# Kernel optimization log

Hardware: AMD Instinct MI355X
Metric: run time of the kernel (lower is better)

Reference implementation:

```python
import jax, jax.numpy as jnp
import numpy as np

CD_WEIGHT = 1.0
EMD_WEIGHT = 1.0
EPS = 1e-3        # sinkhorn entropic regularization (matches eps=0.001)
ITERS = 50        # matches max_iters=50 (stop_thresh ignored: fixed trip count for jit)
NEG = -1e9        # log(0) stand-in for padded points
BIG = 1e10        # +inf stand-in for masked chamfer distances


def _sqdist(x, y):
    # x [N,3], y [M,3] -> squared euclidean distances [N,M]  (p=2 cost)
    return jnp.maximum(
        jnp.sum(x * x, -1)[:, None] + jnp.sum(y * y, -1)[None, :] - 2.0 * (x @ y.T),
        0.0,
    )


def _sinkhorn_cost(x, y, n, m):
    # Log-domain Sinkhorn OT cost between one padded pair: x [N,3], y [M,3],
    # with n, m valid points and uniform marginals 1/n, 1/m on valid points.
    N, M = x.shape[0], y.shape[0]
    C = _sqdist(x, y)
    nf = n.astype(jnp.float32)
    mf = m.astype(jnp.float32)
    log_a = jnp.where(jnp.arange(N) < n, -jnp.log(nf), NEG)  # [N]
    log_b = jnp.where(jnp.arange(M) < m, -jnp.log(mf), NEG)  # [M]

    def body(_, fg):
        f, g = fg
        f = -EPS * jax.scipy.special.logsumexp(log_b[None, :] + (g[None, :] - C) / EPS, axis=1)
        g = -EPS * jax.scipy.special.logsumexp(log_a[:, None] + (f[:, None] - C) / EPS, axis=0)
        return (f, g)

    f, g = jax.lax.fori_loop(0, ITERS, body, (jnp.zeros(N), jnp.zeros(M)))
    log_P = log_a[:, None] + log_b[None, :] + (f[:, None] + g[None, :] - C) / EPS
    return jnp.sum(jnp.exp(log_P) * C)


def _chamfer(px, gy, n_len, m_len):
    # pytorch3d chamfer_distance with point_reduction='mean', batch_reduction='mean'
    # px [B,N,3], gy [B,M,3]; n_len/m_len [B] float valid counts.
    B, N, _ = px.shape
    M = gy.shape[1]
    D = jnp.maximum(
        jnp.sum(px * px, -1)[:, :, None]
        + jnp.sum(gy * gy, -1)[:, None, :]
        - 2.0 * jnp.einsum('bnd,bmd->bnm', px, gy),
        0.0,
    )  # [B,N,M]
    mx = jnp.arange(N)[None, :] < n_len[:, None]  # [B,N]
    my = jnp.arange(M)[None, :] < m_len[:, None]  # [B,M]
    dx = jnp.min(jnp.where(my[:, None, :], D, BIG), axis=2)  # [B,N] NN dist x->y
    dy = jnp.min(jnp.where(mx[:, :, None], D, BIG), axis=1)  # [B,M] NN dist y->x
    cham_x = jnp.sum(jnp.where(mx, dx, 0.0), axis=1) / n_len.astype(jnp.float32)
    cham_y = jnp.sum(jnp.where(my, dy, 0.0), axis=1) / m_len.astype(jnp.float32)
    return jnp.mean(cham_x + cham_y)


def setup_inputs() -> dict:
    key = jax.random.key(0)
    k1, k2, k3, k4 = jax.random.split(key, 4)
    B, N, M = 8, 2048, 2048
    pred_points = 0.5 * jax.random.normal(k1, (B, N, 3), dtype=jnp.float32)
    gt_points = 0.5 * jax.random.normal(k2, (B, M, 3), dtype=jnp.float32)
    pred_lengths = jax.random.randint(k3, (B,), N // 2, N + 1, dtype=jnp.int32)
    gt_lengths = jax.random.randint(k4, (B,), M // 2, M + 1, dtype=jnp.int32)
    return {
        'pred_points': pred_points,
        'gt_points': gt_points,
        'pred_lengths': pred_lengths,
        'gt_lengths': gt_lengths,
    }


def reference(pred_points, gt_points, pred_lengths, gt_lengths):
    # Original clips extracted points to [-1, 1] before losses.
    px = jnp.clip(pred_points, -1.0, 1.0)
    gy = jnp.clip(gt_points, -1.0, 1.0)
    # EMD: per-sample sinkhorn cost, sqrt, mean over samples, weighted.
    emd_costs = jax.vmap(_sinkhorn_cost)(px, gy, pred_lengths, gt_lengths)  # [B]
    emd_loss = EMD_WEIGHT * jnp.mean(jnp.sqrt(emd_costs))
    # Chamfer on padded clouds with lengths.
    cd_loss = CD_WEIGHT * _chamfer(px, gy, pred_lengths.astype(jnp.float32), gt_lengths.astype(jnp.float32))
    return cd_loss + emd_loss
```

## Files before the change

### kernel.cpp

```cpp
#include <hip/hip_runtime.h>

#define BATCH 8
#define NPTS  2048
#define TPB   512
#define WGB   64
#define NWG   (BATCH*WGB)
#define ITERS 50
#define R     4

#define KLOG2E    1442.6950408889634f
#define TWO_K     2885.3900817779268f
#define INV_TK    3.4657359027997264e-4f
#define INV_K     6.931471805599453e-4f
#define INV_2K_SQ 1.2011325347955035e-7f
#define AR_SCALE  -1.7328679513998632e-4f
#define EPS_LN2   6.931471805599453e-4f
#define LN2       0.6931471805599453f
#define EPSV      1e-3f
#define NEGU      -1e30f
#define BIGD      1e10f

__device__ __forceinline__ float exp2fast(float x) { return __builtin_amdgcn_exp2f(x); }
__device__ __forceinline__ float log2fast(float x) { return __builtin_amdgcn_logf(x); }
__device__ __forceinline__ float clipf(float v)    { return fminf(fmaxf(v, -1.0f), 1.0f); }

__device__ __forceinline__ float aloadf(const float* p) {
    return __hip_atomic_load(p, __ATOMIC_RELAXED, __HIP_MEMORY_SCOPE_AGENT);
}
__device__ __forceinline__ void astoref(float* p, float v) {
    __hip_atomic_store(p, v, __ATOMIC_RELAXED, __HIP_MEMORY_SCOPE_AGENT);
}
__device__ __forceinline__ int aloadi(const int* p) {
    return __hip_atomic_load(p, __ATOMIC_RELAXED, __HIP_MEMORY_SCOPE_AGENT);
}

__device__ __forceinline__ float wsum(float v) {
#pragma unroll
    for (int d = 1; d < 64; d <<= 1) v += __shfl_xor(v, d);
    return v;
}
__device__ __forceinline__ float wmax(float v) {
#pragma unroll
    for (int d = 1; d < 64; d <<= 1) v = fmaxf(v, __shfl_xor(v, d));
    return v;
}
__device__ __forceinline__ float wmin(float v) {
#pragma unroll
    for (int d = 1; d < 64; d <<= 1) v = fminf(v, __shfl_xor(v, d));
    return v;
}

__device__ __forceinline__ void batch_barrier(int* cnt, int* gen, int tid)
{
    __syncthreads();
    if (tid == 0) {
        asm volatile("s_waitcnt vmcnt(0)" ::: "memory");
        int g = aloadi(gen);
        int a = __hip_atomic_fetch_add(cnt, 1, __ATOMIC_RELAXED, __HIP_MEMORY_SCOPE_AGENT);
        if (a == WGB - 1) {
            __hip_atomic_store(cnt, 0, __ATOMIC_RELAXED, __HIP_MEMORY_SCOPE_AGENT);
            asm volatile("s_waitcnt vmcnt(0)" ::: "memory");
            __hip_atomic_store(gen, g + 1, __ATOMIC_RELAXED, __HIP_MEMORY_SCOPE_AGENT);
        } else {
            while (aloadi(gen) == g) __builtin_amdgcn_s_sleep(1);
        }
    }
    __syncthreads();
}

__device__ __forceinline__ void half_fused(const float4* __restrict__ colbuf,
                                           const float4* __restrict__ rowbuf,
                                           float* __restrict__ outv,
                                           float* L, float* D,
                                           int nrows, int ncols, float eln,
                                           int r0, int lane)
{
    if (r0 >= nrows) return;
    const int nst = (ncols + 63) >> 6;
    const float4* cb = colbuf + lane;

    float x0[R], x1[R], x2[R], ar[R], Lp[R];
#pragma unroll
    for (int r = 0; r < R; ++r) {
        float4 s = rowbuf[r0 + r];
        x0[r] = s.x * INV_TK; x1[r] = s.y * INV_TK; x2[r] = s.z * INV_TK;
        ar[r] = AR_SCALE * fmaf(s.x, s.x, fmaf(s.y, s.y, s.z * s.z));
        Lp[r] = L[r] + D[r];
    }

    float S[R];
#pragma unroll
    for (int r = 0; r < R; ++r) S[r] = 0.0f;
#pragma unroll 2
    for (int s = 0; s < nst; ++s) {
        float4 yb = cb[s << 6];
#pragma unroll
        for (int r = 0; r < R; ++r) {
            float t = fmaf(x0[r], yb.x, fmaf(x1[r], yb.y, fmaf(x2[r], yb.z, yb.w)));
            S[r] += exp2fast(t - Lp[r]);
        }
    }
    float Ssum[R];
    bool redo = false;
#pragma unroll
    for (int r = 0; r < R; ++r) {
        Ssum[r] = wsum(S[r]);
        redo |= !(Ssum[r] >= 1e-30f && Ssum[r] <= 1e30f);
    }
    if (redo) {
        float Mn[R];
#pragma unroll
        for (int r = 0; r < R; ++r) Mn[r] = -3.0e38f;
        for (int s = 0; s < nst; ++s) {
            float4 yb = cb[s << 6];
#pragma unroll
            for (int r = 0; r < R; ++r) {
                float t = fmaf(x0[r], yb.x, fmaf(x1[r], yb.y, fmaf(x2[r], yb.z, yb.w)));
                Mn[r] = fmaxf(Mn[r], t);
            }
        }
#pragma unroll
        for (int r = 0; r < R; ++r) { Lp[r] = wmax(Mn[r]); S[r] = 0.0f; }
        for (int s = 0; s < nst; ++s) {
            float4 yb = cb[s << 6];
#pragma unroll
            for (int r = 0; r < R; ++r) {
                float t = fmaf(x0[r], yb.x, fmaf(x1[r], yb.y, fmaf(x2[r], yb.z, yb.w)));
                S[r] += exp2fast(t - Lp[r]);
            }
        }
#pragma unroll
        for (int r = 0; r < R; ++r) Ssum[r] = wsum(S[r]);
    }

    float fv[R];
#pragma unroll
    for (int r = 0; r < R; ++r) {
        float lnew = Lp[r] + log2fast(Ssum[r]);
        D[r] = (L[r] > 1.0e37f) ? 0.0f : (lnew - L[r]);
        L[r] = lnew;
        fv[r] = fmaf(-EPS_LN2, ar[r] + lnew, eln);
    }
    float v = fv[0];
#pragma unroll
    for (int r = 1; r < R; ++r) v = (lane == r) ? fv[r] : v;
    if (lane < R && (r0 + lane) < nrows) astoref(&outv[r0 + lane], v);
}

__launch_bounds__(TPB, 4)
__global__ void pcl_kernel(const float* __restrict__ pred,
                           const float* __restrict__ gt,
                           const int* __restrict__ nlen,
                           const int* __restrict__ mlen,
                           int* __restrict__ hdr,
                           float* __restrict__ fbuf,
                           float* __restrict__ gbuf,
                           float* __restrict__ parts,
                           float* __restrict__ bres,
                           float* __restrict__ out)
{
    __shared__ float4 xbuf[NPTS];
    __shared__ float4 ybuf[NPTS];

    const int tid  = threadIdx.x;
    const int wg   = blockIdx.x;
    const int lo   = wg & 255;
    const int hi   = wg >> 8;
    const int b    = ((lo & 7) + hi) & 7;
    const int wloc = (lo >> 3) + hi * 32;
    const int wv   = tid >> 6;
    const int lane = tid & 63;
    const int r0   = wloc * 32 + wv * R;
    const int n = nlen[b];
    const int m = mlen[b];
    const float nf = (float)n, mf = (float)m;
    const float* predb = pred + (size_t)b * NPTS * 3;
    const float* gtb   = gt   + (size_t)b * NPTS * 3;
    float* fb = fbuf + b * NPTS;
    float* gb = gbuf + b * NPTS;
    int* cnt  = hdr + b * 16;
    int* gen  = hdr + 128 + b * 16;
    int* done = hdr + 256;

    for (int idx = tid; idx < NPTS; idx += TPB) {
        const float* p = predb + (size_t)idx * 3;
        xbuf[idx] = make_float4(clipf(p[0]) * TWO_K, clipf(p[1]) * TWO_K, clipf(p[2]) * TWO_K, 0.0f);
        const float* q = gtb + (size_t)idx * 3;
        ybuf[idx] = make_float4(clipf(q[0]) * TWO_K, clipf(q[1]) * TWO_K, clipf(q[2]) * TWO_K, 0.0f);
    }

    const float eln_m = EPSV * LN2 * log2fast(mf);
    const float eln_n = EPSV * LN2 * log2fast(nf);

    float Lf[R], Lg[R], Df[R], Dg[R];
#pragma unroll
    for (int r = 0; r < R; ++r) {
        Lf[r] = 3.0e38f; Lg[r] = 3.0e38f;
        Df[r] = 0.0f;    Dg[r] = 0.0f;
    }

    for (int it = 0; it < ITERS; ++it) {
        for (int j = tid; j < NPTS; j += TPB) {
            float4 yb = ybuf[j];
            float yy = fmaf(yb.x, yb.x, fmaf(yb.y, yb.y, yb.z * yb.z)) * INV_2K_SQ;
            float gval = (it == 0) ? 0.0f : aloadf(&gb[j]);
            ybuf[j].w = (j < m) ? (gval - yy) * KLOG2E : NEGU;
        }
        __syncthreads();
        half_fused(ybuf, xbuf, fb, Lf, Df, n, m, eln_m, r0, lane);
        batch_barrier(cnt, gen, tid);
        for (int i = tid; i < NPTS; i += TPB) {
            float4 xb = xbuf[i];
            float xx = fmaf(xb.x, xb.x, fmaf(xb.y, xb.y, xb.z * xb.z)) * INV_2K_SQ;
            xbuf[i].w = (i < n) ? (aloadf(&fb[i]) - xx) * KLOG2E : NEGU;
        }
        __syncthreads();
        half_fused(xbuf, ybuf, gb, Lg, Dg, m, n, eln_n, r0, lane);
        batch_barrier(cnt, gen, tid);
    }

    for (int j = tid; j < NPTS; j += TPB) {
        float4 yb = ybuf[j];
        float yy = fmaf(yb.x, yb.x, fmaf(yb.y, yb.y, yb.z * yb.z)) * INV_2K_SQ;
        ybuf[j].w = (j < m) ? (aloadf(&gb[j]) - yy) * KLOG2E : NEGU;
    }
    __syncthreads();

    float wcost = 0.0f, chx = 0.0f;
    if (r0 < n) {
        float px0[R], px1[R], px2[R], pxx[R], hrow[R], dmn[R];
#pragma unroll
        for (int r = 0; r < R; ++r) {
            float4 s = xbuf[r0 + r];
            px0[r] = s.x * INV_TK; px1[r] = s.y * INV_TK; px2[r] = s.z * INV_TK;
            pxx[r] = fmaf(s.x, s.x, fmaf(s.y, s.y, s.z * s.z)) * INV_2K_SQ;
            hrow[r] = (r0 + r < n) ? (aloadf(&fb[r0 + r]) - pxx[r]) * KLOG2E : NEGU;
            dmn[r] = BIGD;
        }
        const int nst = (m + 63) >> 6;
#pragma unroll 2
        for (int s = 0; s < nst; ++s) {
            int jj = (s << 6) + lane;
            float4 yb = ybuf[jj];
            float yy = fmaf(yb.x, yb.x, fmaf(yb.y, yb.y, yb.z * yb.z)) * INV_2K_SQ;
            bool jv = jj < m;
#pragma unroll
            for (int r = 0; r < R; ++r) {
                float dots = fmaf(px0[r], yb.x, fmaf(px1[r], yb.y, px2[r] * yb.z));
                float e = hrow[r] + yb.w + dots;
                float w = exp2fast(e);
                float C = fmaxf(fmaf(dots, -INV_K, pxx[r] + yy), 0.0f);
                wcost = fmaf(w, C, wcost);
                dmn[r] = fminf(dmn[r], jv ? C : BIGD);
            }
        }
#pragma unroll
        for (int r = 0; r < R; ++r) {
            float d = wmin(dmn[r]);
            if (r0 + r < n) chx += d;
        }
        wcost = wsum(wcost);
    }

    float chy = 0.0f;
    if (r0 < m) {
        float qy0[R], qy1[R], qy2[R], qyy[R], dmn[R];
#pragma unroll
        for (int r = 0; r < R; ++r) {
            float4 s = ybuf[r0 + r];
            qy0[r] = s.x * INV_TK; qy1[r] = s.y * INV_TK; qy2[r] = s.z * INV_TK;
            qyy[r] = fmaf(s.x, s.x, fmaf(s.y, s.y, s.z * s.z)) * INV_2K_SQ;
            dmn[r] = BIGD;
        }
        const int nst = (n + 63) >> 6;
#pragma unroll 2
        for (int s = 0; s < nst; ++s) {
            int ii = (s << 6) + lane;
            float4 xb = xbuf[ii];
            float xx = fmaf(xb.x, xb.x, fmaf(xb.y, xb.y, xb.z * xb.z)) * INV_2K_SQ;
            bool iv = ii < n;
#pragma unroll
            for (int r = 0; r < R; ++r) {
                float dots = fmaf(qy0[r], xb.x, fmaf(qy1[r], xb.y, qy2[r] * xb.z));
                float C = fmaxf(fmaf(dots, -INV_K, qyy[r] + xx), 0.0f);
                dmn[r] = fminf(dmn[r], iv ? C : BIGD);
            }
        }
#pragma unroll
        for (int r = 0; r < R; ++r) {
            float d = wmin(dmn[r]);
            if (r0 + r < m) chy += d;
        }
    }
    __syncthreads();

    float* xs = (float*)xbuf;
    if (lane == 0) { xs[wv] = wcost; xs[8 + wv] = chx; xs[16 + wv] = chy; }
    __syncthreads();
    if (tid == 0) {
        float cs = 0.0f, cx = 0.0f, cy = 0.0f;
        for (int w = 0; w < 8; ++w) { cs += xs[w]; cx += xs[8 + w]; cy += xs[16 + w]; }
        astoref(&parts[(b * WGB + wloc) * 4 + 0], cs);
        astoref(&parts[(b * WGB + wloc) * 4 + 1], cx);
        astoref(&parts[(b * WGB + wloc) * 4 + 2], cy);
    }
    batch_barrier(cnt, gen, tid);

    if (wloc == 0 && wv == 0) {
        float cs = aloadf(&parts[(b * WGB + lane) * 4 + 0]);
        float cx = aloadf(&parts[(b * WGB + lane) * 4 + 1]);
        float cy = aloadf(&parts[(b * WGB + lane) * 4 + 2]);
        cs = wsum(cs); cx = wsum(cx); cy = wsum(cy);
        if (lane == 0) {
            float cost = cs / (nf * mf);
            astoref(&bres[b], sqrtf(fmaxf(cost, 0.0f)) + cx / nf + cy / mf);
            asm volatile("s_waitcnt vmcnt(0)" ::: "memory");
            int a = __hip_atomic_fetch_add(done, 1, __ATOMIC_RELAXED, __HIP_MEMORY_SCOPE_AGENT);
            if (a == BATCH - 1) {
                float acc = 0.0f;
                for (int i2 = 0; i2 < BATCH; ++i2) acc += aloadf(&bres[i2]);
                out[0] = acc * 0.125f;
            }
        }
    }
}

extern "C" void kernel_launch(void* const* d_in, const int* in_sizes, int n_in,
                              void* d_out, int out_size, void* d_ws, size_t ws_size,
                              hipStream_t stream) {
    const float* pred = (const float*)d_in[0];
    const float* gt   = (const float*)d_in[1];
    const int*  nlen  = (const int*)d_in[2];
    const int*  mlen  = (const int*)d_in[3];

    int*   hdr   = (int*)d_ws;
    float* base  = (float*)d_ws + 512;
    float* fbuf  = base;
    float* gbuf  = fbuf + BATCH * NPTS;
    float* parts = gbuf + BATCH * NPTS;
    float* bres  = parts + NWG * 4;
    float* out   = (float*)d_out;

    hipMemsetAsync(d_ws, 0, 2048, stream);
    hipLaunchKernelGGL(pcl_kernel, dim3(NWG), dim3(TPB), 0, stream,
                       pred, gt, nlen, mlen, hdr, fbuf, gbuf, parts, bres, out);
}
```

Measured before the change: 835.9 us.

## Use packed FP32 math with SoA shared layout and hierarchical batch barrier

Shared point buffers move from float4 AoS to split x/y/z/w arrays of float2, so the inner Sinkhorn loop can use v_pk_fma_f32/v_pk_add_f32 and handle two columns per lane per step. The dual potentials are now stored directly in the log2-scaled domain, which drops the per-iteration rescaling of the column weights. The per-batch grid barrier becomes a two-level tree (8 sub-counters feeding a top counter) to cut contention on a single atomic. Chamfer loops are also converted to paired-column processing. The risks are inline asm that blocks compiler scheduling, higher register pressure, and a more complex barrier.

```diff
diff --git a/kernel.cpp b/kernel.cpp
--- a/kernel.cpp
+++ b/kernel.cpp
@@ -14,15 +14,26 @@
 #define INV_K     6.931471805599453e-4f
 #define INV_2K_SQ 1.2011325347955035e-7f
 #define AR_SCALE  -1.7328679513998632e-4f
-#define EPS_LN2   6.931471805599453e-4f
-#define LN2       0.6931471805599453f
-#define EPSV      1e-3f
 #define NEGU      -1e30f
 #define BIGD      1e10f
+
+typedef float f2 __attribute__((ext_vector_type(2)));
 
 __device__ __forceinline__ float exp2fast(float x) { return __builtin_amdgcn_exp2f(x); }
 __device__ __forceinline__ float log2fast(float x) { return __builtin_amdgcn_logf(x); }
 __device__ __forceinline__ float clipf(float v)    { return fminf(fmaxf(v, -1.0f), 1.0f); }
+__device__ __forceinline__ f2 bc(float x) { f2 r; r.x = x; r.y = x; return r; }
+
+__device__ __forceinline__ f2 pk_fma(f2 a, f2 b, f2 c) {
+    f2 d;
+    asm("v_pk_fma_f32 %0, %1, %2, %3" : "=v"(d) : "v"(a), "v"(b), "v"(c));
+    return d;
+}
+__device__ __forceinline__ f2 pk_add(f2 a, f2 b) {
+    f2 d;
+    asm("v_pk_add_f32 %0, %1, %2" : "=v"(d) : "v"(a), "v"(b));
+    return d;
+}
 
 __device__ __forceinline__ float aloadf(const float* p) {
     return __hip_atomic_load(p, __ATOMIC_RELAXED, __HIP_MEMORY_SCOPE_AGENT);
@@ -33,6 +44,9 @@
 __device__ __forceinline__ int aloadi(const int* p) {
     return __hip_atomic_load(p, __ATOMIC_RELAXED, __HIP_MEMORY_SCOPE_AGENT);
 }
+__device__ __forceinline__ void astorei(int* p, int v) {
+    __hip_atomic_store(p, v, __ATOMIC_RELAXED, __HIP_MEMORY_SCOPE_AGENT);
+}
 
 __device__ __forceinline__ float wsum(float v) {
 #pragma unroll
@@ -50,17 +64,25 @@
     return v;
 }
 
-__device__ __forceinline__ void batch_barrier(int* cnt, int* gen, int tid)
+__device__ __forceinline__ void batch_barrier(int* subs_base, int* sub, int* top,
+                                              int* gen, int tid)
 {
     __syncthreads();
     if (tid == 0) {
         asm volatile("s_waitcnt vmcnt(0)" ::: "memory");
         int g = aloadi(gen);
-        int a = __hip_atomic_fetch_add(cnt, 1, __ATOMIC_RELAXED, __HIP_MEMORY_SCOPE_AGENT);
-        if (a == WGB - 1) {
-            __hip_atomic_store(cnt, 0, __ATOMIC_RELAXED, __HIP_MEMORY_SCOPE_AGENT);
-            asm volatile("s_waitcnt vmcnt(0)" ::: "memory");
-            __hip_atomic_store(gen, g + 1, __ATOMIC_RELAXED, __HIP_MEMORY_SCOPE_AGENT);
+        int a = __hip_atomic_fetch_add(sub, 1, __ATOMIC_RELAXED, __HIP_MEMORY_SCOPE_AGENT);
+        if (a == 7) {
+            int t = __hip_atomic_fetch_add(top, 1, __ATOMIC_RELAXED, __HIP_MEMORY_SCOPE_AGENT);
+            if (t == 7) {
+#pragma unroll
+                for (int s = 0; s < 8; ++s) astorei(subs_base + s * 16, 0);
+                astorei(top, 0);
+                asm volatile("s_waitcnt vmcnt(0)" ::: "memory");
+                astorei(gen, g + 1);
+            } else {
+                while (aloadi(gen) == g) __builtin_amdgcn_s_sleep(1);
+            }
         } else {
             while (aloadi(gen) == g) __builtin_amdgcn_s_sleep(1);
         }
@@ -68,43 +90,51 @@
     __syncthreads();
 }
 
-__device__ __forceinline__ void half_fused(const float4* __restrict__ colbuf,
-                                           const float4* __restrict__ rowbuf,
-                                           float* __restrict__ outv,
-                                           float* L, float* D,
-                                           int nrows, int ncols, float eln,
-                                           int r0, int lane)
+__device__ __forceinline__ void half_fused_pk(
+    const f2* __restrict__ cx, const f2* __restrict__ cy,
+    const f2* __restrict__ cz, const f2* __restrict__ cw,
+    const f2* __restrict__ rx, const f2* __restrict__ ry, const f2* __restrict__ rz,
+    float* __restrict__ uout, float L2C, float* L, float* D,
+    int nrows, int ncols, int r0, int lane)
 {
     if (r0 >= nrows) return;
-    const int nst = (ncols + 63) >> 6;
-    const float4* cb = colbuf + lane;
-
-    float x0[R], x1[R], x2[R], ar[R], Lp[R];
-#pragma unroll
-    for (int r = 0; r < R; ++r) {
-        float4 s = rowbuf[r0 + r];
-        x0[r] = s.x * INV_TK; x1[r] = s.y * INV_TK; x2[r] = s.z * INV_TK;
-        ar[r] = AR_SCALE * fmaf(s.x, s.x, fmaf(s.y, s.y, s.z * s.z));
-        Lp[r] = L[r] + D[r];
-    }
-
-    float S[R];
-#pragma unroll
-    for (int r = 0; r < R; ++r) S[r] = 0.0f;
-#pragma unroll 2
+    const int nst = (ncols + 127) >> 7;
+    const int rp = r0 >> 1;
+    f2 vx0 = rx[rp], vx1 = rx[rp + 1];
+    f2 vy0 = ry[rp], vy1 = ry[rp + 1];
+    f2 vz0 = rz[rp], vz1 = rz[rp + 1];
+    f2 x0p[R] = { bc(vx0.x * INV_TK), bc(vx0.y * INV_TK), bc(vx1.x * INV_TK), bc(vx1.y * INV_TK) };
+    f2 x1p[R] = { bc(vy0.x * INV_TK), bc(vy0.y * INV_TK), bc(vy1.x * INV_TK), bc(vy1.y * INV_TK) };
+    f2 x2p[R] = { bc(vz0.x * INV_TK), bc(vz0.y * INV_TK), bc(vz1.x * INV_TK), bc(vz1.y * INV_TK) };
+
+    float Lp[R];
+    f2 nLp[R];
+#pragma unroll
+    for (int r = 0; r < R; ++r) { Lp[r] = L[r] + D[r]; nLp[r] = bc(-Lp[r]); }
+
+    float S0[R], S1[R];
+#pragma unroll
+    for (int r = 0; r < R; ++r) { S0[r] = 0.0f; S1[r] = 0.0f; }
+
     for (int s = 0; s < nst; ++s) {
-        float4 yb = cb[s << 6];
-#pragma unroll
-        for (int r = 0; r < R; ++r) {
-            float t = fmaf(x0[r], yb.x, fmaf(x1[r], yb.y, fmaf(x2[r], yb.z, yb.w)));
-            S[r] += exp2fast(t - Lp[r]);
-        }
-    }
+        int p = (s << 6) + lane;
+        f2 bx = cx[p], by = cy[p], bz = cz[p], bw = cw[p];
+#pragma unroll
+        for (int r = 0; r < R; ++r) {
+            f2 t = pk_fma(x2p[r], bz, bw);
+            t = pk_fma(x1p[r], by, t);
+            t = pk_fma(x0p[r], bx, t);
+            t = pk_add(nLp[r], t);
+            S0[r] += exp2fast(t.x);
+            S1[r] += exp2fast(t.y);
+        }
+    }
+
     float Ssum[R];
     bool redo = false;
 #pragma unroll
     for (int r = 0; r < R; ++r) {
-        Ssum[r] = wsum(S[r]);
+        Ssum[r] = wsum(S0[r] + S1[r]);
         redo |= !(Ssum[r] >= 1e-30f && Ssum[r] <= 1e30f);
     }
     if (redo) {
@@ -112,39 +142,50 @@
 #pragma unroll
         for (int r = 0; r < R; ++r) Mn[r] = -3.0e38f;
         for (int s = 0; s < nst; ++s) {
-            float4 yb = cb[s << 6];
+            int p = (s << 6) + lane;
+            f2 bx = cx[p], by = cy[p], bz = cz[p], bw = cw[p];
 #pragma unroll
             for (int r = 0; r < R; ++r) {
-                float t = fmaf(x0[r], yb.x, fmaf(x1[r], yb.y, fmaf(x2[r], yb.z, yb.w)));
-                Mn[r] = fmaxf(Mn[r], t);
-            }
-        }
-#pragma unroll
-        for (int r = 0; r < R; ++r) { Lp[r] = wmax(Mn[r]); S[r] = 0.0f; }
+                f2 t = pk_fma(x2p[r], bz, bw);
+                t = pk_fma(x1p[r], by, t);
+                t = pk_fma(x0p[r], bx, t);
+                Mn[r] = fmaxf(Mn[r], fmaxf(t.x, t.y));
+            }
+        }
+#pragma unroll
+        for (int r = 0; r < R; ++r) {
+            Lp[r] = wmax(Mn[r]); nLp[r] = bc(-Lp[r]);
+            S0[r] = 0.0f; S1[r] = 0.0f;
+        }
         for (int s = 0; s < nst; ++s) {
-            float4 yb = cb[s << 6];
+            int p = (s << 6) + lane;
+            f2 bx = cx[p], by = cy[p], bz = cz[p], bw = cw[p];
 #pragma unroll
             for (int r = 0; r < R; ++r) {
-                float t = fmaf(x0[r], yb.x, fmaf(x1[r], yb.y, fmaf(x2[r], yb.z, yb.w)));
-                S[r] += exp2fast(t - Lp[r]);
-            }
-        }
-#pragma unroll
-        for (int r = 0; r < R; ++r) Ssum[r] = wsum(S[r]);
-    }
-
-    float fv[R];
+                f2 t = pk_fma(x2p[r], bz, bw);
+                t = pk_fma(x1p[r], by, t);
+                t = pk_fma(x0p[r], bx, t);
+                t = pk_add(nLp[r], t);
+                S0[r] += exp2fast(t.x);
+                S1[r] += exp2fast(t.y);
+            }
+        }
+#pragma unroll
+        for (int r = 0; r < R; ++r) Ssum[r] = wsum(S0[r] + S1[r]);
+    }
+
+    float uv[R];
 #pragma unroll
     for (int r = 0; r < R; ++r) {
         float lnew = Lp[r] + log2fast(Ssum[r]);
         D[r] = (L[r] > 1.0e37f) ? 0.0f : (lnew - L[r]);
         L[r] = lnew;
-        fv[r] = fmaf(-EPS_LN2, ar[r] + lnew, eln);
-    }
-    float v = fv[0];
-#pragma unroll
-    for (int r = 1; r < R; ++r) v = (lane == r) ? fv[r] : v;
-    if (lane < R && (r0 + lane) < nrows) astoref(&outv[r0 + lane], v);
+        uv[r] = L2C - lnew;
+    }
+    float v = uv[0];
+#pragma unroll
+    for (int r = 1; r < R; ++r) v = (lane == r) ? uv[r] : v;
+    if (lane < R && (r0 + lane) < nrows) astoref(&uout[r0 + lane], v);
 }
 
 __launch_bounds__(TPB, 4)
@@ -159,8 +200,8 @@
                            float* __restrict__ bres,
                            float* __restrict__ out)
 {
-    __shared__ float4 xbuf[NPTS];
-    __shared__ float4 ybuf[NPTS];
+    __shared__ f2 XSX[NPTS/2], XSY[NPTS/2], XSZ[NPTS/2], XSW[NPTS/2];
+    __shared__ f2 YSX[NPTS/2], YSY[NPTS/2], YSZ[NPTS/2], YSW[NPTS/2];
 
     const int tid  = threadIdx.x;
     const int wg   = blockIdx.x;
@@ -178,19 +219,26 @@
     const float* gtb   = gt   + (size_t)b * NPTS * 3;
     float* fb = fbuf + b * NPTS;
     float* gb = gbuf + b * NPTS;
-    int* cnt  = hdr + b * 16;
-    int* gen  = hdr + 128 + b * 16;
-    int* done = hdr + 256;
+    int* subs_base = hdr + b * 128;
+    int* sub       = subs_base + (wloc >> 3) * 16;
+    int* top       = hdr + (64 + b) * 16;
+    int* gen       = hdr + (72 + b) * 16;
+    int* done      = hdr + 80 * 16;
 
     for (int idx = tid; idx < NPTS; idx += TPB) {
         const float* p = predb + (size_t)idx * 3;
-        xbuf[idx] = make_float4(clipf(p[0]) * TWO_K, clipf(p[1]) * TWO_K, clipf(p[2]) * TWO_K, 0.0f);
+        ((float*)XSX)[idx] = clipf(p[0]) * TWO_K;
+        ((float*)XSY)[idx] = clipf(p[1]) * TWO_K;
+        ((float*)XSZ)[idx] = clipf(p[2]) * TWO_K;
         const float* q = gtb + (size_t)idx * 3;
-        ybuf[idx] = make_float4(clipf(q[0]) * TWO_K, clipf(q[1]) * TWO_K, clipf(q[2]) * TWO_K, 0.0f);
-    }
-
-    const float eln_m = EPSV * LN2 * log2fast(mf);
-    const float eln_n = EPSV * LN2 * log2fast(nf);
+        ((float*)YSX)[idx] = clipf(q[0]) * TWO_K;
+        ((float*)YSY)[idx] = clipf(q[1]) * TWO_K;
+        ((float*)YSZ)[idx] = clipf(q[2]) * TWO_K;
+    }
+    __syncthreads();
+
+    const float L2M = log2fast(mf);
+    const float L2N = log2fast(nf);
 
     float Lf[R], Lg[R], Df[R], Dg[R];
 #pragma unroll
@@ -200,63 +248,71 @@
     }
 
     for (int it = 0; it < ITERS; ++it) {
-        for (int j = tid; j < NPTS; j += TPB) {
-            float4 yb = ybuf[j];
-            float yy = fmaf(yb.x, yb.x, fmaf(yb.y, yb.y, yb.z * yb.z)) * INV_2K_SQ;
-            float gval = (it == 0) ? 0.0f : aloadf(&gb[j]);
-            ybuf[j].w = (j < m) ? (gval - yy) * KLOG2E : NEGU;
+        if (it == 0) {
+            for (int j = tid; j < NPTS; j += TPB) {
+                float sx = ((float*)YSX)[j], sy = ((float*)YSY)[j], sz = ((float*)YSZ)[j];
+                float u0 = AR_SCALE * fmaf(sx, sx, fmaf(sy, sy, sz * sz));
+                ((float*)YSW)[j] = (j < m) ? u0 : NEGU;
+            }
+        } else {
+            for (int j = tid; j < NPTS; j += TPB)
+                ((float*)YSW)[j] = (j < m) ? aloadf(&gb[j]) : NEGU;
         }
         __syncthreads();
-        half_fused(ybuf, xbuf, fb, Lf, Df, n, m, eln_m, r0, lane);
-        batch_barrier(cnt, gen, tid);
-        for (int i = tid; i < NPTS; i += TPB) {
-            float4 xb = xbuf[i];
-            float xx = fmaf(xb.x, xb.x, fmaf(xb.y, xb.y, xb.z * xb.z)) * INV_2K_SQ;
-            xbuf[i].w = (i < n) ? (aloadf(&fb[i]) - xx) * KLOG2E : NEGU;
-        }
+        half_fused_pk(YSX, YSY, YSZ, YSW, XSX, XSY, XSZ, fb, L2M, Lf, Df, n, m, r0, lane);
+        batch_barrier(subs_base, sub, top, gen, tid);
+        for (int i = tid; i < NPTS; i += TPB)
+            ((float*)XSW)[i] = (i < n) ? aloadf(&fb[i]) : NEGU;
         __syncthreads();
-        half_fused(xbuf, ybuf, gb, Lg, Dg, m, n, eln_n, r0, lane);
-        batch_barrier(cnt, gen, tid);
-    }
-
-    for (int j = tid; j < NPTS; j += TPB) {
-        float4 yb = ybuf[j];
-        float yy = fmaf(yb.x, yb.x, fmaf(yb.y, yb.y, yb.z * yb.z)) * INV_2K_SQ;
-        ybuf[j].w = (j < m) ? (aloadf(&gb[j]) - yy) * KLOG2E : NEGU;
-    }
+        half_fused_pk(XSX, XSY, XSZ, XSW, YSX, YSY, YSZ, gb, L2N, Lg, Dg, m, n, r0, lane);
+        batch_barrier(subs_base, sub, top, gen, tid);
+    }
+
+    for (int j = tid; j < NPTS; j += TPB)
+        ((float*)YSW)[j] = (j < m) ? aloadf(&gb[j]) : NEGU;
     __syncthreads();
 
     float wcost = 0.0f, chx = 0.0f;
     if (r0 < n) {
-        float px0[R], px1[R], px2[R], pxx[R], hrow[R], dmn[R];
-#pragma unroll
-        for (int r = 0; r < R; ++r) {
-            float4 s = xbuf[r0 + r];
-            px0[r] = s.x * INV_TK; px1[r] = s.y * INV_TK; px2[r] = s.z * INV_TK;
-            pxx[r] = fmaf(s.x, s.x, fmaf(s.y, s.y, s.z * s.z)) * INV_2K_SQ;
-            hrow[r] = (r0 + r < n) ? (aloadf(&fb[r0 + r]) - pxx[r]) * KLOG2E : NEGU;
-            dmn[r] = BIGD;
-        }
-        const int nst = (m + 63) >> 6;
-#pragma unroll 2
+        const int rp = r0 >> 1;
+        f2 vx0 = XSX[rp], vx1 = XSX[rp + 1];
+        f2 vy0 = XSY[rp], vy1 = XSY[rp + 1];
+        f2 vz0 = XSZ[rp], vz1 = XSZ[rp + 1];
+        float px0[R] = { vx0.x * INV_TK, vx0.y * INV_TK, vx1.x * INV_TK, vx1.y * INV_TK };
+        float px1[R] = { vy0.x * INV_TK, vy0.y * INV_TK, vy1.x * INV_TK, vy1.y * INV_TK };
+        float px2[R] = { vz0.x * INV_TK, vz0.y * INV_TK, vz1.x * INV_TK, vz1.y * INV_TK };
+        float pxx[R], hrow[R];
+        f2 dmn[R];
+#pragma unroll
+        for (int r = 0; r < R; ++r) {
+            float sx = px0[r] * TWO_K, sy = px1[r] * TWO_K, sz = px2[r] * TWO_K;
+            pxx[r] = fmaf(sx, sx, fmaf(sy, sy, sz * sz)) * INV_2K_SQ;
+            hrow[r] = (r0 + r < n) ? aloadf(&fb[r0 + r]) : NEGU;
+            dmn[r].x = BIGD; dmn[r].y = BIGD;
+        }
+        const int nst = (m + 127) >> 7;
         for (int s = 0; s < nst; ++s) {
-            int jj = (s << 6) + lane;
-            float4 yb = ybuf[jj];
-            float yy = fmaf(yb.x, yb.x, fmaf(yb.y, yb.y, yb.z * yb.z)) * INV_2K_SQ;
-            bool jv = jj < m;
+            int p = (s << 6) + lane;
+            f2 bx = YSX[p], by = YSY[p], bz = YSZ[p], bw = YSW[p];
+            f2 yy2 = (bx * bx + by * by + bz * bz) * INV_2K_SQ;
+            bool jv0 = (2 * p)     < m;
+            bool jv1 = (2 * p + 1) < m;
 #pragma unroll
             for (int r = 0; r < R; ++r) {
-                float dots = fmaf(px0[r], yb.x, fmaf(px1[r], yb.y, px2[r] * yb.z));
-                float e = hrow[r] + yb.w + dots;
-                float w = exp2fast(e);
-                float C = fmaxf(fmaf(dots, -INV_K, pxx[r] + yy), 0.0f);
-                wcost = fmaf(w, C, wcost);
-                dmn[r] = fminf(dmn[r], jv ? C : BIGD);
-            }
-        }
-#pragma unroll
-        for (int r = 0; r < R; ++r) {
-            float d = wmin(dmn[r]);
+                f2 dots = px0[r] * bx + px1[r] * by + px2[r] * bz;
+                f2 e = dots + bw + hrow[r];
+                float w0 = exp2fast(e.x), w1 = exp2fast(e.y);
+                f2 C;
+                C.x = fmaxf(fmaf(dots.x, -INV_K, pxx[r] + yy2.x), 0.0f);
+                C.y = fmaxf(fmaf(dots.y, -INV_K, pxx[r] + yy2.y), 0.0f);
+                wcost = fmaf(w0, C.x, fmaf(w1, C.y, wcost));
+                dmn[r].x = fminf(dmn[r].x, jv0 ? C.x : BIGD);
+                dmn[r].y = fminf(dmn[r].y, jv1 ? C.y : BIGD);
+            }
+        }
+#pragma unroll
+        for (int r = 0; r < R; ++r) {
+            float d = wmin(fminf(dmn[r].x, dmn[r].y));
             if (r0 + r < n) chx += d;
         }
         wcost = wsum(wcost);
@@ -264,37 +320,47 @@
 
     float chy = 0.0f;
     if (r0 < m) {
-        float qy0[R], qy1[R], qy2[R], qyy[R], dmn[R];
-#pragma unroll
-        for (int r = 0; r < R; ++r) {
-            float4 s = ybuf[r0 + r];
-            qy0[r] = s.x * INV_TK; qy1[r] = s.y * INV_TK; qy2[r] = s.z * INV_TK;
-            qyy[r] = fmaf(s.x, s.x, fmaf(s.y, s.y, s.z * s.z)) * INV_2K_SQ;
-            dmn[r] = BIGD;
-        }
-        const int nst = (n + 63) >> 6;
-#pragma unroll 2
+        const int rp = r0 >> 1;
+        f2 vx0 = YSX[rp], vx1 = YSX[rp + 1];
+        f2 vy0 = YSY[rp], vy1 = YSY[rp + 1];
+        f2 vz0 = YSZ[rp], vz1 = YSZ[rp + 1];
+        float qy0[R] = { vx0.x * INV_TK, vx0.y * INV_TK, vx1.x * INV_TK, vx1.y * INV_TK };
+        float qy1[R] = { vy0.x * INV_TK, vy0.y * INV_TK, vy1.x * INV_TK, vy1.y * INV_TK };
+        float qy2[R] = { vz0.x * INV_TK, vz0.y * INV_TK, vz1.x * INV_TK, vz1.y * INV_TK };
+        float qyy[R];
+        f2 dmn[R];
+#pragma unroll
+        for (int r = 0; r < R; ++r) {
+            float sx = qy0[r] * TWO_K, sy = qy1[r] * TWO_K, sz = qy2[r] * TWO_K;
+            qyy[r] = fmaf(sx, sx, fmaf(sy, sy, sz * sz)) * INV_2K_SQ;
+            dmn[r].x = BIGD; dmn[r].y = BIGD;
+        }
+        const int nst = (n + 127) >> 7;
         for (int s = 0; s < nst; ++s) {
-            int ii = (s << 6) + lane;
-            float4 xb = xbuf[ii];
-            float xx = fmaf(xb.x, xb.x, fmaf(xb.y, xb.y, xb.z * xb.z)) * INV_2K_SQ;
-            bool iv = ii < n;
+            int p = (s << 6) + lane;
+            f2 bx = XSX[p], by = XSY[p], bz = XSZ[p];
+            f2 xx2 = (bx * bx + by * by + bz * bz) * INV_2K_SQ;
+            bool iv0 = (2 * p)     < n;
+            bool iv1 = (2 * p + 1) < n;
 #pragma unroll
             for (int r = 0; r < R; ++r) {
-                float dots = fmaf(qy0[r], xb.x, fmaf(qy1[r], xb.y, qy2[r] * xb.z));
-                float C = fmaxf(fmaf(dots, -INV_K, qyy[r] + xx), 0.0f);
-                dmn[r] = fminf(dmn[r], iv ? C : BIGD);
-            }
-        }
-#pragma unroll
-        for (int r = 0; r < R; ++r) {
-            float d = wmin(dmn[r]);
+                f2 dots = qy0[r] * bx + qy1[r] * by + qy2[r] * bz;
+                f2 C;
+                C.x = fmaxf(fmaf(dots.x, -INV_K, qyy[r] + xx2.x), 0.0f);
+                C.y = fmaxf(fmaf(dots.y, -INV_K, qyy[r] + xx2.y), 0.0f);
+                dmn[r].x = fminf(dmn[r].x, iv0 ? C.x : BIGD);
+                dmn[r].y = fminf(dmn[r].y, iv1 ? C.y : BIGD);
+            }
+        }
+#pragma unroll
+        for (int r = 0; r < R; ++r) {
+            float d = wmin(fminf(dmn[r].x, dmn[r].y));
             if (r0 + r < m) chy += d;
         }
     }
     __syncthreads();
 
-    float* xs = (float*)xbuf;
+    float* xs = (float*)XSX;
     if (lane == 0) { xs[wv] = wcost; xs[8 + wv] = chx; xs[16 + wv] = chy; }
     __syncthreads();
     if (tid == 0) {
@@ -304,7 +370,7 @@
         astoref(&parts[(b * WGB + wloc) * 4 + 1], cx);
         astoref(&parts[(b * WGB + wloc) * 4 + 2], cy);
     }
-    batch_barrier(cnt, gen, tid);
+    batch_barrier(subs_base, sub, top, gen, tid);
 
     if (wloc == 0 && wv == 0) {
         float cs = aloadf(&parts[(b * WGB + lane) * 4 + 0]);
@@ -334,14 +400,14 @@
     const int*  mlen  = (const int*)d_in[3];
 
     int*   hdr   = (int*)d_ws;
-    float* base  = (float*)d_ws + 512;
+    float* base  = (float*)d_ws + 2048;
     float* fbuf  = base;
     float* gbuf  = fbuf + BATCH * NPTS;
     float* parts = gbuf + BATCH * NPTS;
     float* bres  = parts + NWG * 4;
     float* out   = (float*)d_out;
 
-    hipMemsetAsync(d_ws, 0, 2048, stream);
+    hipMemsetAsync(d_ws, 0, 8192, stream);
     hipLaunchKernelGGL(pcl_kernel, dim3(NWG), dim3(TPB), 0, stream,
                        pred, gt, nlen, mlen, hdr, fbuf, gbuf, parts, bres, out);
 }
```

Result: faster. 806.2 us (-3.6%).
